# Performance work log

Hardware: AMD Instinct MI355X
Metric: run time of the kernel (lower is better)

Reference implementation:

```python
import jax, jax.numpy as jnp
import numpy as np

N, E, IN, H, C = 50000, 800000, 128, 256, 2
EPS = 1e-5


def setup_inputs() -> dict:
    key = jax.random.key(0)
    ks = jax.random.split(key, 12)
    inp = {
        "x": jax.random.normal(ks[0], (N, IN), jnp.float32),
        "edge_index": jax.random.randint(ks[1], (2, E), 0, N, jnp.int32),
        "w_nei0": jax.random.normal(ks[2], (IN, H), jnp.float32) * 0.05,
        "w_root0": jax.random.normal(ks[3], (IN, H), jnp.float32) * 0.05,
        "b0": jnp.zeros((H,), jnp.float32),
        "w_nei": jax.random.normal(ks[4], (2, H, H), jnp.float32) * 0.05,
        "w_root": jax.random.normal(ks[5], (2, H, H), jnp.float32) * 0.05,
        "b": jnp.zeros((2, H), jnp.float32),
        "bn_gamma": jnp.ones((3, H), jnp.float32),
        "bn_beta": jnp.zeros((3, H), jnp.float32),
        "bn_mean": jax.random.normal(ks[6], (3, H), jnp.float32) * 0.05,
        "bn_var": jnp.ones((3, H), jnp.float32),
        "w1": jax.random.normal(ks[7], (H, H // 2), jnp.float32) * 0.05,
        "b1": jnp.zeros((H // 2,), jnp.float32),
        "w2": jax.random.normal(ks[8], (H // 2, C), jnp.float32) * 0.05,
        "b2": jnp.zeros((C,), jnp.float32),
    }
    return inp


def _mean_aggregate(h, src, dst, inv_deg):
    # gather source-node features, scatter-sum to destinations, divide by degree
    agg = jax.ops.segment_sum(h[src], dst, num_segments=N)  # (N, d)
    return agg * inv_deg[:, None]


def _forward(x, edge_index, w_nei0, w_root0, b0, w_nei, w_root, b,
             bn_gamma, bn_beta, bn_mean, bn_var, w1, b1, w2, b2):
    src, dst = edge_index[0], edge_index[1]
    deg = jax.ops.segment_sum(jnp.ones((E,), x.dtype), dst, num_segments=N)
    inv_deg = 1.0 / jnp.maximum(deg, 1.0)

    h = x
    wn_list = [w_nei0, w_nei[0], w_nei[1]]
    wr_list = [w_root0, w_root[0], w_root[1]]
    bias_list = [b0, b[0], b[1]]
    for i in range(3):
        mean_nb = _mean_aggregate(h, src, dst, inv_deg)          # (N, d_in)
        h = mean_nb @ wn_list[i] + bias_list[i] + h @ wr_list[i]  # SAGEConv
        # BatchNorm1d (eval: running stats) + ReLU; dropout is identity in eval
        h = (h - bn_mean[i]) * jax.lax.rsqrt(bn_var[i] + EPS) * bn_gamma[i] + bn_beta[i]
        h = jax.nn.relu(h)

    h = jax.nn.relu(h @ w1 + b1)
    logits = h @ w2 + b2
    return jax.nn.log_softmax(logits, axis=1)


def reference(x, edge_index, w_nei0, w_root0, b0, w_nei, w_root, b,
              bn_gamma, bn_beta, bn_mean, bn_var, w1, b1, w2, b2):
    return _forward(x, edge_index, w_nei0, w_root0, b0, w_nei, w_root, b,
                    bn_gamma, bn_beta, bn_mean, bn_var, w1, b1, w2, b2)
```

## Files before the change

kernel.cpp:

```cpp
#include <hip/hip_runtime.h>
#include <hip/hip_fp16.h>

#define N_NODES 50000
#define N_EDGES 800000
#define DIM_IN 128
#define DIM_H 256

typedef _Float16 f16;
typedef _Float16 half8 __attribute__((ext_vector_type(8)));
typedef _Float16 f16x4 __attribute__((ext_vector_type(4)));
typedef _Float16 f16x2 __attribute__((ext_vector_type(2)));
typedef float f32x4 __attribute__((ext_vector_type(4)));
typedef unsigned int u32;

__device__ __forceinline__ void gload_lds16(const void* g, void* l) {
    __builtin_amdgcn_global_load_lds(
        (const __attribute__((address_space(1))) u32*)g,
        (__attribute__((address_space(3))) u32*)l,
        16, 0, 0);
}


__global__ void k_deg(const int* __restrict__ dst, int* __restrict__ deg) {
    int i = blockIdx.x * 256 + threadIdx.x;
    if (i < N_EDGES) atomicAdd(&deg[dst[i]], 1);
}

__global__ void k_scan1(const int* __restrict__ deg, int* __restrict__ row_start,
                        int* __restrict__ partials) {
    __shared__ int sm[256];
    int t = threadIdx.x;
    int i = blockIdx.x * 256 + t;
    int v = (i < N_NODES) ? deg[i] : 0;
    sm[t] = v;
    __syncthreads();
    for (int ofs = 1; ofs < 256; ofs <<= 1) {
        int add = (t >= ofs) ? sm[t - ofs] : 0;
        __syncthreads();
        sm[t] += add;
        __syncthreads();
    }
    if (i < N_NODES) row_start[i] = sm[t] - v;
    if (t == 255) partials[blockIdx.x] = sm[255];
}

__global__ void k_scan2(const int* __restrict__ partials, int* __restrict__ pscan, int nblk) {
    __shared__ int sm[256];
    int t = threadIdx.x;
    int v = (t < nblk) ? partials[t] : 0;
    sm[t] = v;
    __syncthreads();
    for (int ofs = 1; ofs < 256; ofs <<= 1) {
        int add = (t >= ofs) ? sm[t - ofs] : 0;
        __syncthreads();
        sm[t] += add;
        __syncthreads();
    }
    pscan[t] = sm[t] - v;
}

__global__ void k_scan3(const int* __restrict__ deg, int* __restrict__ row_start,
                        const int* __restrict__ pscan, float* __restrict__ inv_deg) {
    int i = blockIdx.x * 256 + threadIdx.x;
    if (i < N_NODES) {
        row_start[i] += pscan[blockIdx.x];
        int d = deg[i];
        inv_deg[i] = 1.0f / (float)(d > 1 ? d : 1);
        if (i == 0) row_start[N_NODES] = N_EDGES;
    }
}

__global__ void k_fill(const int* __restrict__ src, const int* __restrict__ dst,
                       const int* __restrict__ row_start, int* __restrict__ cursor,
                       int* __restrict__ csr) {
    int i = blockIdx.x * 256 + threadIdx.x;
    if (i < N_EDGES) {
        int d = dst[i];
        int p = atomicAdd(&cursor[d], 1);
        csr[row_start[d] + p] = src[i];
    }
}


__global__ void k_cvt_x(const float* __restrict__ x, f16* __restrict__ o) {
    int i = blockIdx.x * 256 + threadIdx.x;
    if (i < N_NODES * DIM_IN / 4) {
        float4 v = ((const float4*)x)[i];
        f16x4 h = {(f16)v.x, (f16)v.y, (f16)v.z, (f16)v.w};
        *(f16x4*)(o + (size_t)i * 4) = h;
    }
}

__global__ void k_tcvt(const float* __restrict__ W, f16* __restrict__ Wt, int K, int NN) {
    int t = blockIdx.x * 256 + threadIdx.x;
    if (t < K * NN) {
        int n = t / K, k = t - n * K;
        Wt[t] = (f16)W[(size_t)k * NN + n];
    }
}

__global__ void k_st(const float* __restrict__ b0, const float* __restrict__ bvec,
                     const float* __restrict__ gamma, const float* __restrict__ beta,
                     const float* __restrict__ mean, const float* __restrict__ var,
                     const float* __restrict__ b1, float* __restrict__ st) {
    int c = threadIdx.x;
    for (int layer = 0; layer < 3; layer++) {
        float bias = (layer == 0) ? b0[c] : bvec[(layer - 1) * DIM_H + c];
        float g = gamma[layer * DIM_H + c];
        float be = beta[layer * DIM_H + c];
        float mu = mean[layer * DIM_H + c];
        float va = var[layer * DIM_H + c];
        float s = g * rsqrtf(va + 1e-5f);
        st[layer * 512 + c] = s;
        st[layer * 512 + 256 + c] = (bias - mu) * s + be;
    }
    st[3 * 512 + c] = 1.0f;
    st[3 * 512 + 256 + c] = (c < 128) ? b1[c] : 0.0f;
}


__global__ void k_agg128(const f16* __restrict__ h, const int* __restrict__ row_start,
                         const int* __restrict__ csr, const float* __restrict__ inv_deg,
                         f16* __restrict__ agg) {
    int wid = threadIdx.x >> 6;
    int lane = threadIdx.x & 63;
    int v = blockIdx.x * 4 + wid;
    if (v >= N_NODES) return;
    int e0 = row_start[v], e1 = row_start[v + 1];
    float acc[2] = {0.0f, 0.0f};

    const int li = lane & 15;
    for (int e = e0; e < e1; e += 16) {
        int ee = e + li;
        int idx = csr[ee < e1 ? ee : e1 - 1];
        int rem = e1 - e;
        f16x2 hv[16];
#pragma unroll
        for (int j = 0; j < 16; j++) {
            int s = __shfl(idx, j);
            hv[j] = *(const f16x2*)(h + (size_t)s * 128 + lane * 2);
        }
#pragma unroll
        for (int j = 0; j < 16; j++) {
            if (j < rem) { acc[0] += (float)hv[j][0]; acc[1] += (float)hv[j][1]; }
        }
    }

    float sc = inv_deg[v];
    f16x2 o = {(f16)(acc[0] * sc), (f16)(acc[1] * sc)};
    *(f16x2*)(agg + (size_t)v * 128 + lane * 2) = o;
}


__global__ void k_agg256(const f16* __restrict__ h, const int* __restrict__ row_start,
                         const int* __restrict__ csr, const float* __restrict__ inv_deg,
                         f16* __restrict__ agg) {
    int wid = threadIdx.x >> 6;
    int lane = threadIdx.x & 63;
    int v = blockIdx.x * 2 + (wid >> 1);
    int half = wid & 1;
    if (v >= N_NODES) return;
    int e0 = row_start[v], e1 = row_start[v + 1];
    float acc[2] = {0.0f, 0.0f};

    const f16* hb = h + half * 128 + lane * 2;
    const int li = lane & 15;
    for (int e = e0; e < e1; e += 16) {
        int ee = e + li;
        int idx = csr[ee < e1 ? ee : e1 - 1];
        int rem = e1 - e;
        f16x2 hv[16];
#pragma unroll
        for (int j = 0; j < 16; j++) {
            int s = __shfl(idx, j);
            hv[j] = *(const f16x2*)(hb + (size_t)s * 256);
        }
#pragma unroll
        for (int j = 0; j < 16; j++) {
            if (j < rem) { acc[0] += (float)hv[j][0]; acc[1] += (float)hv[j][1]; }
        }
    }

    float sc = inv_deg[v];
    f16x2 o = {(f16)(acc[0] * sc), (f16)(acc[1] * sc)};
    *(f16x2*)(agg + (size_t)v * 256 + half * 128 + lane * 2) = o;
}


__global__ __launch_bounds__(256) void k_gemm(
    const f16* __restrict__ A1, int lda1, const f16* __restrict__ B1, int k1,
    const f16* __restrict__ A2, int lda2, const f16* __restrict__ B2, int k2,
    const float* __restrict__ sc, const float* __restrict__ sh,
    f16* __restrict__ out, int ldo, int M) {
    __shared__ f16 aT[2][128 * 32];
    __shared__ f16 bT[2][128 * 32];
    const int tid = threadIdx.x;
    const int lane = tid & 63;
    const int wid = tid >> 6;
    const int wm = wid >> 1, wn = wid & 1;
    const int m0 = blockIdx.x * 128;
    const int n0 = blockIdx.y * 128;
    f32x4 acc[4][4] = {};

    const int srow = tid >> 2;
    const int schunk = (tid & 3) ^ ((tid >> 3) & 3);
    const int ktot = k1 + k2;

    auto stage = [&](int buf, int kk) {
        const f16 *Ap, *Bp;
        int lda, ldb, kloc;
        if (kk < k1) { Ap = A1; Bp = B1; lda = lda1; ldb = k1; kloc = kk; }
        else         { Ap = A2; Bp = B2; lda = lda2; ldb = k2; kloc = kk - k1; }
#pragma unroll
        for (int hh = 0; hh < 2; hh++) {
            int r = hh * 64 + srow;
            int gm = m0 + r;
            gm = gm < M ? gm : M - 1;
            gload_lds16(Ap + (size_t)gm * lda + kloc + schunk * 8,
                        (char*)&aT[buf][0] + hh * 4096 + tid * 16);
            gload_lds16(Bp + (size_t)(n0 + r) * ldb + kloc + schunk * 8,
                        (char*)&bT[buf][0] + hh * 4096 + tid * 16);
        }
    };

    auto compute = [&](int buf) {
        half8 af[4], bf[4];
#pragma unroll
        for (int mi = 0; mi < 4; mi++) {
            int row = wm * 64 + mi * 16 + (lane & 15);
            int ch = (lane >> 4) ^ ((row >> 1) & 3);
            af[mi] = *(const half8*)((const char*)&aT[buf][0] + row * 64 + ch * 16);
        }
#pragma unroll
        for (int ni = 0; ni < 4; ni++) {
            int row = wn * 64 + ni * 16 + (lane & 15);
            int ch = (lane >> 4) ^ ((row >> 1) & 3);
            bf[ni] = *(const half8*)((const char*)&bT[buf][0] + row * 64 + ch * 16);
        }
#pragma unroll
        for (int mi = 0; mi < 4; mi++)
#pragma unroll
            for (int ni = 0; ni < 4; ni++)
                acc[mi][ni] = __builtin_amdgcn_mfma_f32_16x16x32_f16(af[mi], bf[ni],
                                                                     acc[mi][ni], 0, 0, 0);
    };

    stage(0, 0);
    __syncthreads();
    int cur = 0;
    for (int kk = 32; kk < ktot; kk += 32) {
        stage(cur ^ 1, kk);
        compute(cur);
        __syncthreads();
        cur ^= 1;
    }
    compute(cur);

#pragma unroll
    for (int mi = 0; mi < 4; mi++) {
#pragma unroll
        for (int ni = 0; ni < 4; ni++) {
            int gcol = n0 + wn * 64 + ni * 16 + (lane & 15);
            float s = sc[gcol], t = sh[gcol];
#pragma unroll
            for (int r = 0; r < 4; r++) {
                int grow = m0 + wm * 64 + mi * 16 + (lane >> 4) * 4 + r;
                if (grow < M) {
                    float val = fmaxf(acc[mi][ni][r] * s + t, 0.0f);
                    out[(size_t)grow * ldo + gcol] = (f16)val;
                }
            }
        }
    }
}


__global__ __launch_bounds__(256) void k_gemm_head(
    const f16* __restrict__ A1, int k1, const f16* __restrict__ B1,
    const float* __restrict__ sh,
    const float* __restrict__ w2, const float* __restrict__ b2,
    float* __restrict__ out, int M) {
    __shared__ f16 aT[2][128 * 32];
    __shared__ f16 bT[2][128 * 32];
    __shared__ float smred[128][2][2];
    const int tid = threadIdx.x;
    const int lane = tid & 63;
    const int wid = tid >> 6;
    const int wm = wid >> 1, wn = wid & 1;
    const int m0 = blockIdx.x * 128;
    f32x4 acc[4][4] = {};

    const int srow = tid >> 2;
    const int schunk = (tid & 3) ^ ((tid >> 3) & 3);

    auto stage = [&](int buf, int kk) {
#pragma unroll
        for (int hh = 0; hh < 2; hh++) {
            int r = hh * 64 + srow;
            int gm = m0 + r;
            gm = gm < M ? gm : M - 1;
            gload_lds16(A1 + (size_t)gm * k1 + kk + schunk * 8,
                        (char*)&aT[buf][0] + hh * 4096 + tid * 16);
            gload_lds16(B1 + (size_t)r * k1 + kk + schunk * 8,
                        (char*)&bT[buf][0] + hh * 4096 + tid * 16);
        }
    };

    auto compute = [&](int buf) {
        half8 af[4], bf[4];
#pragma unroll
        for (int mi = 0; mi < 4; mi++) {
            int row = wm * 64 + mi * 16 + (lane & 15);
            int ch = (lane >> 4) ^ ((row >> 1) & 3);
            af[mi] = *(const half8*)((const char*)&aT[buf][0] + row * 64 + ch * 16);
        }
#pragma unroll
        for (int ni = 0; ni < 4; ni++) {
            int row = wn * 64 + ni * 16 + (lane & 15);
            int ch = (lane >> 4) ^ ((row >> 1) & 3);
            bf[ni] = *(const half8*)((const char*)&bT[buf][0] + row * 64 + ch * 16);
        }
#pragma unroll
        for (int mi = 0; mi < 4; mi++)
#pragma unroll
            for (int ni = 0; ni < 4; ni++)
                acc[mi][ni] = __builtin_amdgcn_mfma_f32_16x16x32_f16(af[mi], bf[ni],
                                                                     acc[mi][ni], 0, 0, 0);
    };

    stage(0, 0);
    __syncthreads();
    int cur = 0;
    for (int kk = 32; kk < k1; kk += 32) {
        stage(cur ^ 1, kk);
        compute(cur);
        __syncthreads();
        cur ^= 1;
    }
    compute(cur);

    float w2c[4][2], shc[4];
#pragma unroll
    for (int ni = 0; ni < 4; ni++) {
        int c = wn * 64 + ni * 16 + (lane & 15);
        w2c[ni][0] = w2[c * 2];
        w2c[ni][1] = w2[c * 2 + 1];
        shc[ni] = sh[c];
    }
#pragma unroll
    for (int mi = 0; mi < 4; mi++) {
#pragma unroll
        for (int r = 0; r < 4; r++) {
            float p0 = 0.0f, p1 = 0.0f;
#pragma unroll
            for (int ni = 0; ni < 4; ni++) {
                float val = fmaxf(acc[mi][ni][r] + shc[ni], 0.0f);
                p0 += val * w2c[ni][0];
                p1 += val * w2c[ni][1];
            }
#pragma unroll
            for (int o = 1; o < 16; o <<= 1) {
                p0 += __shfl_xor(p0, o);
                p1 += __shfl_xor(p1, o);
            }
            if ((lane & 15) == 0) {
                int lrow = wm * 64 + mi * 16 + (lane >> 4) * 4 + r;
                smred[lrow][wn][0] = p0;
                smred[lrow][wn][1] = p1;
            }
        }
    }
    __syncthreads();
    if (tid < 128) {
        int grow = m0 + tid;
        if (grow < M) {
            float l0 = smred[tid][0][0] + smred[tid][1][0] + b2[0];
            float l1 = smred[tid][0][1] + smred[tid][1][1] + b2[1];
            float m = fmaxf(l0, l1);
            float lse = m + logf(expf(l0 - m) + expf(l1 - m));
            out[(size_t)grow * 2] = l0 - lse;
            out[(size_t)grow * 2 + 1] = l1 - lse;
        }
    }
}


extern "C" void kernel_launch(void* const* d_in, const int* in_sizes, int n_in,
                              void* d_out, int out_size, void* d_ws, size_t ws_size,
                              hipStream_t stream) {
    const float* x     = (const float*)d_in[0];
    const int*   ei    = (const int*)d_in[1];
    const float* wn0   = (const float*)d_in[2];
    const float* wr0   = (const float*)d_in[3];
    const float* b0    = (const float*)d_in[4];
    const float* wn12  = (const float*)d_in[5];
    const float* wr12  = (const float*)d_in[6];
    const float* bvec  = (const float*)d_in[7];
    const float* gamma = (const float*)d_in[8];
    const float* beta  = (const float*)d_in[9];
    const float* mean  = (const float*)d_in[10];
    const float* var   = (const float*)d_in[11];
    const float* w1    = (const float*)d_in[12];
    const float* b1    = (const float*)d_in[13];
    const float* w2    = (const float*)d_in[14];
    const float* b2    = (const float*)d_in[15];
    const int* srcv = ei;
    const int* dstv = ei + N_EDGES;

    char* p = (char*)d_ws;
    auto alloc = [&](size_t bytes) {
        char* r = p;
        p += (bytes + 255) & ~(size_t)255;
        return r;
    };
    int*   deg       = (int*)alloc((size_t)N_NODES * 4);
    int*   row_start = (int*)alloc((size_t)(N_NODES + 1) * 4);
    int*   cursor    = (int*)alloc((size_t)N_NODES * 4);
    float* inv_deg   = (float*)alloc((size_t)N_NODES * 4);
    int*   partials  = (int*)alloc(256 * 4);
    int*   pscan     = (int*)alloc(256 * 4);
    int*   csr       = (int*)alloc((size_t)N_EDGES * 4);
    f16*   Wn0t      = (f16*)alloc(128 * 256 * 2);
    f16*   Wr0t      = (f16*)alloc(128 * 256 * 2);
    f16*   Wn1t      = (f16*)alloc(256 * 256 * 2);
    f16*   Wr1t      = (f16*)alloc(256 * 256 * 2);
    f16*   Wn2t      = (f16*)alloc(256 * 256 * 2);
    f16*   Wr2t      = (f16*)alloc(256 * 256 * 2);
    f16*   W1t       = (f16*)alloc(256 * 128 * 2);
    float* st        = (float*)alloc(4 * 512 * 4);
    f16*   hA        = (f16*)alloc((size_t)N_NODES * 256 * 2);
    f16*   hB        = (f16*)alloc((size_t)N_NODES * 256 * 2);
    f16*   agg       = (f16*)alloc((size_t)N_NODES * 256 * 2);

    hipMemsetAsync(deg, 0, (size_t)N_NODES * 4, stream);
    hipMemsetAsync(cursor, 0, (size_t)N_NODES * 4, stream);

    const int EB = (N_EDGES + 255) / 256;
    const int NBLK = (N_NODES + 255) / 256;
    k_deg<<<EB, 256, 0, stream>>>(dstv, deg);
    k_scan1<<<NBLK, 256, 0, stream>>>(deg, row_start, partials);
    k_scan2<<<1, 256, 0, stream>>>(partials, pscan, NBLK);
    k_scan3<<<NBLK, 256, 0, stream>>>(deg, row_start, pscan, inv_deg);
    k_fill<<<EB, 256, 0, stream>>>(srcv, dstv, row_start, cursor, csr);

    k_cvt_x<<<(N_NODES * DIM_IN / 4 + 255) / 256, 256, 0, stream>>>(x, hA);
    k_tcvt<<<128, 256, 0, stream>>>(wn0, Wn0t, 128, 256);
    k_tcvt<<<128, 256, 0, stream>>>(wr0, Wr0t, 128, 256);
    k_tcvt<<<256, 256, 0, stream>>>(wn12, Wn1t, 256, 256);
    k_tcvt<<<256, 256, 0, stream>>>(wn12 + 65536, Wn2t, 256, 256);
    k_tcvt<<<256, 256, 0, stream>>>(wr12, Wr1t, 256, 256);
    k_tcvt<<<256, 256, 0, stream>>>(wr12 + 65536, Wr2t, 256, 256);
    k_tcvt<<<128, 256, 0, stream>>>(w1, W1t, 256, 128);
    k_st<<<1, 256, 0, stream>>>(b0, bvec, gamma, beta, mean, var, b1, st);

    const int AB4 = (N_NODES + 3) / 4;
    const int AB2 = (N_NODES + 1) / 2;
    dim3 g2((N_NODES + 127) / 128, 2);

    k_agg128<<<AB4, 256, 0, stream>>>(hA, row_start, csr, inv_deg, agg);
    k_gemm<<<g2, 256, 0, stream>>>(agg, 128, Wn0t, 128, hA, 128, Wr0t, 128,
                                   st + 0, st + 256, hB, 256, N_NODES);
    k_agg256<<<AB2, 256, 0, stream>>>(hB, row_start, csr, inv_deg, agg);
    k_gemm<<<g2, 256, 0, stream>>>(agg, 256, Wn1t, 256, hB, 256, Wr1t, 256,
                                   st + 512, st + 768, hA, 256, N_NODES);
    k_agg256<<<AB2, 256, 0, stream>>>(hA, row_start, csr, inv_deg, agg);
    k_gemm<<<g2, 256, 0, stream>>>(agg, 256, Wn2t, 256, hA, 256, Wr2t, 256,
                                   st + 1024, st + 1280, hB, 256, N_NODES);
    k_gemm_head<<<(N_NODES + 127) / 128, 256, 0, stream>>>(
        hB, 256, W1t, st + 1792, w2, b2, (float*)d_out, N_NODES);
}
```

Before: 397.1 us.

## Use one wave per node in 256-wide aggregation and full-width 64-row GEMM tiles

The aggregation kernels are merged into a template, so each wave now handles a whole node and each lane loads a 4-wide fp16 vector for D=256, not two half-waves with 2-wide loads. This halves the number of index loads and shuffles per node and issues wider memory reads. The GEMM tile changes from 128x128 to 64 rows by the full 256 columns, so each A tile is read once instead of twice across column blocks. The cost is a larger B tile staged in LDS per block and a different occupancy and grid shape.

```diff
diff --git a/kernel.cpp b/kernel.cpp
--- a/kernel.cpp
+++ b/kernel.cpp
@@ -119,71 +119,46 @@
 }
 
 
-__global__ void k_agg128(const f16* __restrict__ h, const int* __restrict__ row_start,
-                         const int* __restrict__ csr, const float* __restrict__ inv_deg,
-                         f16* __restrict__ agg) {
+template <int D>
+__global__ void k_agg(const f16* __restrict__ h, const int* __restrict__ row_start,
+                      const int* __restrict__ csr, const float* __restrict__ inv_deg,
+                      f16* __restrict__ agg) {
+    constexpr int V = D / 64;
+    typedef _Float16 fvec __attribute__((ext_vector_type(V)));
     int wid = threadIdx.x >> 6;
     int lane = threadIdx.x & 63;
     int v = blockIdx.x * 4 + wid;
     if (v >= N_NODES) return;
     int e0 = row_start[v], e1 = row_start[v + 1];
-    float acc[2] = {0.0f, 0.0f};
+    float acc[V];
+#pragma unroll
+    for (int j = 0; j < V; j++) acc[j] = 0.0f;
 
     const int li = lane & 15;
     for (int e = e0; e < e1; e += 16) {
         int ee = e + li;
         int idx = csr[ee < e1 ? ee : e1 - 1];
         int rem = e1 - e;
-        f16x2 hv[16];
+        fvec hv[16];
 #pragma unroll
         for (int j = 0; j < 16; j++) {
             int s = __shfl(idx, j);
-            hv[j] = *(const f16x2*)(h + (size_t)s * 128 + lane * 2);
+            hv[j] = *(const fvec*)(h + (size_t)s * D + lane * V);
         }
 #pragma unroll
         for (int j = 0; j < 16; j++) {
-            if (j < rem) { acc[0] += (float)hv[j][0]; acc[1] += (float)hv[j][1]; }
+            if (j < rem) {
+#pragma unroll
+                for (int q = 0; q < V; q++) acc[q] += (float)hv[j][q];
+            }
         }
     }
 
     float sc = inv_deg[v];
-    f16x2 o = {(f16)(acc[0] * sc), (f16)(acc[1] * sc)};
-    *(f16x2*)(agg + (size_t)v * 128 + lane * 2) = o;
-}
-
-
-__global__ void k_agg256(const f16* __restrict__ h, const int* __restrict__ row_start,
-                         const int* __restrict__ csr, const float* __restrict__ inv_deg,
-                         f16* __restrict__ agg) {
-    int wid = threadIdx.x >> 6;
-    int lane = threadIdx.x & 63;
-    int v = blockIdx.x * 2 + (wid >> 1);
-    int half = wid & 1;
-    if (v >= N_NODES) return;
-    int e0 = row_start[v], e1 = row_start[v + 1];
-    float acc[2] = {0.0f, 0.0f};
-
-    const f16* hb = h + half * 128 + lane * 2;
-    const int li = lane & 15;
-    for (int e = e0; e < e1; e += 16) {
-        int ee = e + li;
-        int idx = csr[ee < e1 ? ee : e1 - 1];
-        int rem = e1 - e;
-        f16x2 hv[16];
-#pragma unroll
-        for (int j = 0; j < 16; j++) {
-            int s = __shfl(idx, j);
-            hv[j] = *(const f16x2*)(hb + (size_t)s * 256);
-        }
-#pragma unroll
-        for (int j = 0; j < 16; j++) {
-            if (j < rem) { acc[0] += (float)hv[j][0]; acc[1] += (float)hv[j][1]; }
-        }
-    }
-
-    float sc = inv_deg[v];
-    f16x2 o = {(f16)(acc[0] * sc), (f16)(acc[1] * sc)};
-    *(f16x2*)(agg + (size_t)v * 256 + half * 128 + lane * 2) = o;
+    fvec o;
+#pragma unroll
+    for (int j = 0; j < V; j++) o[j] = (f16)(acc[j] * sc);
+    *(fvec*)(agg + (size_t)v * D + lane * V) = o;
 }
 
 
@@ -192,14 +167,12 @@
     const f16* __restrict__ A2, int lda2, const f16* __restrict__ B2, int k2,
     const float* __restrict__ sc, const float* __restrict__ sh,
     f16* __restrict__ out, int ldo, int M) {
-    __shared__ f16 aT[2][128 * 32];
-    __shared__ f16 bT[2][128 * 32];
+    __shared__ f16 aT[2][64 * 32];
+    __shared__ f16 bT[2][256 * 32];
     const int tid = threadIdx.x;
     const int lane = tid & 63;
     const int wid = tid >> 6;
-    const int wm = wid >> 1, wn = wid & 1;
-    const int m0 = blockIdx.x * 128;
-    const int n0 = blockIdx.y * 128;
+    const int m0 = blockIdx.x * 64;
     f32x4 acc[4][4] = {};
 
     const int srow = tid >> 2;
@@ -211,14 +184,13 @@
         int lda, ldb, kloc;
         if (kk < k1) { Ap = A1; Bp = B1; lda = lda1; ldb = k1; kloc = kk; }
         else         { Ap = A2; Bp = B2; lda = lda2; ldb = k2; kloc = kk - k1; }
-#pragma unroll
-        for (int hh = 0; hh < 2; hh++) {
-            int r = hh * 64 + srow;
-            int gm = m0 + r;
-            gm = gm < M ? gm : M - 1;
-            gload_lds16(Ap + (size_t)gm * lda + kloc + schunk * 8,
-                        (char*)&aT[buf][0] + hh * 4096 + tid * 16);
-            gload_lds16(Bp + (size_t)(n0 + r) * ldb + kloc + schunk * 8,
+        int gm = m0 + srow;
+        gm = gm < M ? gm : M - 1;
+        gload_lds16(Ap + (size_t)gm * lda + kloc + schunk * 8,
+                    (char*)&aT[buf][0] + tid * 16);
+#pragma unroll
+        for (int hh = 0; hh < 4; hh++) {
+            gload_lds16(Bp + (size_t)(hh * 64 + srow) * ldb + kloc + schunk * 8,
                         (char*)&bT[buf][0] + hh * 4096 + tid * 16);
         }
     };
@@ -227,13 +199,13 @@
         half8 af[4], bf[4];
 #pragma unroll
         for (int mi = 0; mi < 4; mi++) {
-            int row = wm * 64 + mi * 16 + (lane & 15);
+            int row = mi * 16 + (lane & 15);
             int ch = (lane >> 4) ^ ((row >> 1) & 3);
             af[mi] = *(const half8*)((const char*)&aT[buf][0] + row * 64 + ch * 16);
         }
 #pragma unroll
         for (int ni = 0; ni < 4; ni++) {
-            int row = wn * 64 + ni * 16 + (lane & 15);
+            int row = wid * 64 + ni * 16 + (lane & 15);
             int ch = (lane >> 4) ^ ((row >> 1) & 3);
             bf[ni] = *(const half8*)((const char*)&bT[buf][0] + row * 64 + ch * 16);
         }
@@ -260,11 +232,11 @@
     for (int mi = 0; mi < 4; mi++) {
 #pragma unroll
         for (int ni = 0; ni < 4; ni++) {
-            int gcol = n0 + wn * 64 + ni * 16 + (lane & 15);
+            int gcol = wid * 64 + ni * 16 + (lane & 15);
             float s = sc[gcol], t = sh[gcol];
 #pragma unroll
             for (int r = 0; r < 4; r++) {
-                int grow = m0 + wm * 64 + mi * 16 + (lane >> 4) * 4 + r;
+                int grow = m0 + mi * 16 + (lane >> 4) * 4 + r;
                 if (grow < M) {
                     float val = fmaxf(acc[mi][ni][r] * s + t, 0.0f);
                     out[(size_t)grow * ldo + gcol] = (f16)val;
@@ -453,18 +425,17 @@
     k_tcvt<<<128, 256, 0, stream>>>(w1, W1t, 256, 128);
     k_st<<<1, 256, 0, stream>>>(b0, bvec, gamma, beta, mean, var, b1, st);
 
-    const int AB4 = (N_NODES + 3) / 4;
-    const int AB2 = (N_NODES + 1) / 2;
-    dim3 g2((N_NODES + 127) / 128, 2);
-
-    k_agg128<<<AB4, 256, 0, stream>>>(hA, row_start, csr, inv_deg, agg);
-    k_gemm<<<g2, 256, 0, stream>>>(agg, 128, Wn0t, 128, hA, 128, Wr0t, 128,
+    const int AB = (N_NODES + 3) / 4;
+    const int GB = (N_NODES + 63) / 64;
+
+    k_agg<128><<<AB, 256, 0, stream>>>(hA, row_start, csr, inv_deg, agg);
+    k_gemm<<<GB, 256, 0, stream>>>(agg, 128, Wn0t, 128, hA, 128, Wr0t, 128,
                                    st + 0, st + 256, hB, 256, N_NODES);
-    k_agg256<<<AB2, 256, 0, stream>>>(hB, row_start, csr, inv_deg, agg);
-    k_gemm<<<g2, 256, 0, stream>>>(agg, 256, Wn1t, 256, hB, 256, Wr1t, 256,
+    k_agg<256><<<AB, 256, 0, stream>>>(hB, row_start, csr, inv_deg, agg);
+    k_gemm<<<GB, 256, 0, stream>>>(agg, 256, Wn1t, 256, hB, 256, Wr1t, 256,
                                    st + 512, st + 768, hA, 256, N_NODES);
-    k_agg256<<<AB2, 256, 0, stream>>>(hA, row_start, csr, inv_deg, agg);
-    k_gemm<<<g2, 256, 0, stream>>>(agg, 256, Wn2t, 256, hA, 256, Wr2t, 256,
+    k_agg<256><<<AB, 256, 0, stream>>>(hA, row_start, csr, inv_deg, agg);
+    k_gemm<<<GB, 256, 0, stream>>>(agg, 256, Wn2t, 256, hA, 256, Wr2t, 256,
                                    st + 1024, st + 1280, hB, 256, N_NODES);
     k_gemm_head<<<(N_NODES + 127) / 128, 256, 0, stream>>>(
         hB, 256, W1t, st + 1792, w2, b2, (float*)d_out, N_NODES);
```

New measurement: 369.7 us. 6.9% less time.
